# Kernel optimization log

Measured on AMD Instinct MI355X. Metric: run time of the kernel, lower is better.

## Reference

```python
import jax, jax.numpy as jnp
import numpy as np
import math

N_NODES = 50000
N_EDGES = 800000
D = 128        # in_channels == out_channels
H = 8          # num_heads
HD = D // H    # head_dim = 16
ED = 32        # edge_dim


def setup_inputs() -> dict:
    key = jax.random.key(0)
    ks = jax.random.split(key, 16)
    s = 1.0 / math.sqrt(D)
    se = 1.0 / math.sqrt(ED)
    return {
        "x": jax.random.normal(ks[0], (N_NODES, D), jnp.float32),
        "edge_index": jax.random.randint(ks[1], (2, N_EDGES), 0, N_NODES, jnp.int64),
        "edge_attr": jax.random.normal(ks[2], (N_EDGES, ED), jnp.float32),
        "Wq": jax.random.normal(ks[3], (D, D), jnp.float32) * s,
        "bq": jnp.zeros((D,), jnp.float32),
        "Wk": jax.random.normal(ks[4], (D, D), jnp.float32) * s,
        "bk": jnp.zeros((D,), jnp.float32),
        "Wv": jax.random.normal(ks[5], (D, D), jnp.float32) * s,
        "bv": jnp.zeros((D,), jnp.float32),
        "We": jax.random.normal(ks[6], (ED, H), jnp.float32) * se,
        "be": jnp.zeros((H,), jnp.float32),
        "Wo": jax.random.normal(ks[7], (D, D), jnp.float32) * s,
        "bo": jnp.zeros((D,), jnp.float32),
        "gamma": jnp.ones((D,), jnp.float32),
        "beta": jnp.zeros((D,), jnp.float32),
    }


def reference(x, edge_index, edge_attr, Wq, bq, Wk, bk, Wv, bv, We, be, Wo, bo, gamma, beta):
    n = x.shape[0]
    residual = x
    # node-wise projections -> [N, H, HD]
    q = (x @ Wq + bq).reshape(n, H, HD)
    k = (x @ Wk + bk).reshape(n, H, HD)
    v = (x @ Wv + bv).reshape(n, H, HD)
    src = edge_index[0]
    dst = edge_index[1]
    # edge-wise gather + dot-product attention score [E, H]
    score = jnp.einsum('ehd,ehd->eh', q[dst], k[src]) / math.sqrt(HD)
    score = score + edge_attr @ We + be
    # segmented (per-destination-node) stable softmax
    m = jax.ops.segment_max(score, dst, num_segments=n)          # [N, H]
    exp_s = jnp.exp(score - m[dst])                              # [E, H]
    ssum = jax.ops.segment_sum(exp_s, dst, num_segments=n)      # [N, H]
    attn = exp_s / (ssum[dst] + 1e-8)                            # [E, H]
    # weighted message scatter-add
    msg = attn[..., None] * v[src]                               # [E, H, HD]
    out = jax.ops.segment_sum(msg, dst, num_segments=n)          # [N, H, HD]
    out = out.reshape(n, D) @ Wo + bo
    # residual + layer norm (eps=1e-5, as nn.LayerNorm default)
    h = out + residual
    mu = h.mean(-1, keepdims=True)
    var = ((h - mu) ** 2).mean(-1, keepdims=True)
    return (h - mu) / jnp.sqrt(var + 1e-5) * gamma + beta
```

## Files before the change

### kernel.cpp

```cpp
#include <hip/hip_runtime.h>

#define DD 128
#define HH 8
#define HDIM 16
#define EDIM 32
#define CAP 64

typedef short short8_t __attribute__((ext_vector_type(8)));
typedef float f32x4 __attribute__((ext_vector_type(4)));

__device__ inline ushort f2bf(float f) {
    unsigned u = __float_as_uint(f);
    unsigned r = (u + 0x7fffu + ((u >> 16) & 1u)) >> 16;
    return (ushort)r;
}
__device__ inline float bf2f(ushort u) { return __uint_as_float(((unsigned)u) << 16); }

__global__ __launch_bounds__(256) void k_prep_w(
    const float* __restrict__ Wq, const float* __restrict__ Wk,
    const float* __restrict__ Wv, const float* __restrict__ Wo,
    ushort* __restrict__ wt)
{
    __shared__ ushort tw[128][136];
    const float* Ws[4] = {Wq, Wk, Wv, Wo};
    const float* W = Ws[blockIdx.x];
    const int t = threadIdx.x;
    for (int idx = t; idx < DD * DD; idx += 256) {
        int k = idx >> 7, c = idx & 127;
        tw[c][k] = f2bf(W[idx]);
    }
    __syncthreads();
    for (int u = t; u < 2048; u += 256) {
        int col = u >> 4, c8 = (u & 15) * 8;
        *(uint4*)&wt[((size_t)blockIdx.x * 128 + col) * 128 + c8] = *(const uint4*)&tw[col][c8];
    }
}

__global__ __launch_bounds__(256) void k_cvt_x(const float* __restrict__ x, ushort* __restrict__ xb, int total8) {
    int i = blockIdx.x * 256 + threadIdx.x;
    if (i >= total8) return;
    float4 a = *(const float4*)&x[(size_t)i * 8];
    float4 b = *(const float4*)&x[(size_t)i * 8 + 4];
    ushort o[8] = {f2bf(a.x), f2bf(a.y), f2bf(a.z), f2bf(a.w),
                   f2bf(b.x), f2bf(b.y), f2bf(b.z), f2bf(b.w)};
    *(uint4*)&xb[(size_t)i * 8] = *(const uint4*)o;
}

__global__ __launch_bounds__(256) void k_qkv(
    const ushort* __restrict__ xb, const ushort* __restrict__ wt,
    const float* __restrict__ bq, const float* __restrict__ bk, const float* __restrict__ bv,
    ushort* __restrict__ qb, ushort* __restrict__ kv, int N)
{
    __shared__ ushort xs[64][136];
    const int t = threadIdx.x;
    const int base = blockIdx.x * 64;

    for (int u = t; u < 1024; u += 256) {
        int r = u >> 4, c8 = (u & 15) * 8;
        int n = base + r;
        uint4 val = (n < N) ? *(const uint4*)&xb[(size_t)n * DD + c8] : make_uint4(0u, 0u, 0u, 0u);
        *(uint4*)&xs[r][c8] = val;
    }
    __syncthreads();

    const int lane = t & 63, w = t >> 6;
    const int lr = lane & 15, g = lane >> 4;
    const int node = base + w * 16 + lr;
    const bool valid = node < N;

    short8_t xf[4];
    #pragma unroll
    for (int ks = 0; ks < 4; ++ks)
        xf[ks] = *(const short8_t*)&xs[w * 16 + lr][ks * 32 + g * 8];

    const float* biases[3] = {bq, bk, bv};
    #pragma unroll
    for (int m = 0; m < 3; ++m) {
        f32x4 acc[8];
        #pragma unroll
        for (int rt = 0; rt < 8; ++rt) acc[rt] = (f32x4){0.f, 0.f, 0.f, 0.f};
        #pragma unroll
        for (int ks = 0; ks < 4; ++ks) {
            #pragma unroll
            for (int rt = 0; rt < 8; ++rt) {
                short8_t wf = *(const short8_t*)&wt[((size_t)m * 128 + rt * 16 + lr) * 128 + ks * 32 + g * 8];
                acc[rt] = __builtin_amdgcn_mfma_f32_16x16x32_bf16(wf, xf[ks], acc[rt], 0, 0, 0);
            }
        }
        if (valid) {
            #pragma unroll
            for (int rt = 0; rt < 8; ++rt) {
                int col = rt * 16 + g * 4;
                float4 b4 = *(const float4*)&biases[m][col];
                ushort o[4] = {f2bf(acc[rt][0] + b4.x), f2bf(acc[rt][1] + b4.y),
                               f2bf(acc[rt][2] + b4.z), f2bf(acc[rt][3] + b4.w)};
                if (m == 0) *(uint2*)&qb[(size_t)node * DD + col] = *(const uint2*)o;
                else        *(uint2*)&kv[(size_t)node * 256 + (m == 1 ? 0 : 128) + col] = *(const uint2*)o;
            }
        }
    }
}

__global__ __launch_bounds__(256) void k_edge(
    const int* __restrict__ ei, const float* __restrict__ edge_attr,
    const float* __restrict__ We, const float* __restrict__ be,
    int E, int N, int* __restrict__ cnt,
    int2* __restrict__ pe, ushort* __restrict__ escore_e)
{
    __shared__ float wel[EDIM * HH];
    __shared__ float bel[HH];
    int t = threadIdx.x;
    for (int i = t; i < EDIM * HH; i += 256) wel[i] = We[i];
    if (t < HH) bel[t] = be[t];
    __syncthreads();

    int e = blockIdx.x * 256 + t;
    if (e >= E) return;
    int dst = ei[E + e];
    int src = ei[e];

    float acc[HH];
    #pragma unroll
    for (int h = 0; h < HH; ++h) acc[h] = bel[h];
    #pragma unroll
    for (int c = 0; c < EDIM; c += 4) {
        float4 a4 = *(const float4*)&edge_attr[(size_t)e * EDIM + c];
        float av[4] = {a4.x, a4.y, a4.z, a4.w};
        #pragma unroll
        for (int cc = 0; cc < 4; ++cc)
            #pragma unroll
            for (int h = 0; h < HH; ++h)
                acc[h] += av[cc] * wel[(c + cc) * HH + h];
    }
    ushort o[8];
    #pragma unroll
    for (int h = 0; h < HH; ++h) o[h] = f2bf(acc[h]);
    *(uint4*)&escore_e[(size_t)e * 8] = *(const uint4*)o;

    if ((unsigned)dst < (unsigned)N) {
        int pos = atomicAdd(&cnt[dst], 1);
        if (pos < CAP)
            pe[(size_t)dst * CAP + pos] = make_int2(((unsigned)src < (unsigned)N) ? src : 0, e);
    }
}

__global__ __launch_bounds__(256) void k_agg(
    const ushort* __restrict__ qb, const ushort* __restrict__ kv,
    const int* __restrict__ cnt, const int2* __restrict__ pe,
    const ushort* __restrict__ escore_e,
    ushort* __restrict__ aggb, int N)
{
    int node = blockIdx.x * 4 + (threadIdx.x >> 6);
    if (node >= N) return;
    int lane = threadIdx.x & 63;
    int h = lane & 7, j = lane >> 3;

    float qr[HDIM];
    {
        uint4 qa = *(const uint4*)&qb[(size_t)node * DD + h * 16];
        uint4 qc = *(const uint4*)&qb[(size_t)node * DD + h * 16 + 8];
        unsigned ua[4] = {qa.x, qa.y, qa.z, qa.w};
        unsigned ub[4] = {qc.x, qc.y, qc.z, qc.w};
        #pragma unroll
        for (int i = 0; i < 4; ++i) {
            qr[2*i]     = __uint_as_float(ua[i] << 16);
            qr[2*i + 1] = __uint_as_float(ua[i] & 0xffff0000u);
            qr[8 + 2*i]     = __uint_as_float(ub[i] << 16);
            qr[8 + 2*i + 1] = __uint_as_float(ub[i] & 0xffff0000u);
        }
    }

    int deg = cnt[node];
    if (deg > CAP) deg = CAP;
    const size_t base = (size_t)node * CAP;

    float acc[HDIM];
    #pragma unroll
    for (int d = 0; d < HDIM; ++d) acc[d] = 0.f;
    float denom = 0.f;

    int tt = j;
    for (; tt + 8 < deg; tt += 16) {
        int2 r0 = pe[base + tt];
        int2 r1 = pe[base + tt + 8];
        int s0 = r0.x, s1 = r1.x;
        float e0 = bf2f(escore_e[(size_t)r0.y * 8 + h]);
        float e1 = bf2f(escore_e[(size_t)r1.y * 8 + h]);
        const uint4* kp0 = (const uint4*)&kv[(size_t)s0 * 256 + h * 16];
        const uint4* kp1 = (const uint4*)&kv[(size_t)s1 * 256 + h * 16];
        uint4 ka0 = kp0[0], kb0 = kp0[1];
        uint4 ka1 = kp1[0], kb1 = kp1[1];
        const uint4* vp0 = (const uint4*)&kv[(size_t)s0 * 256 + 128 + h * 16];
        const uint4* vp1 = (const uint4*)&kv[(size_t)s1 * 256 + 128 + h * 16];
        uint4 va0 = vp0[0], vb0 = vp0[1];
        uint4 va1 = vp1[0], vb1 = vp1[1];

        float kf0[16], kf1[16], vf0[16], vf1[16];
        {
            unsigned ua[4] = {ka0.x, ka0.y, ka0.z, ka0.w};
            unsigned ub[4] = {kb0.x, kb0.y, kb0.z, kb0.w};
            #pragma unroll
            for (int i = 0; i < 4; ++i) {
                kf0[2*i]     = __uint_as_float(ua[i] << 16);
                kf0[2*i + 1] = __uint_as_float(ua[i] & 0xffff0000u);
                kf0[8 + 2*i]     = __uint_as_float(ub[i] << 16);
                kf0[8 + 2*i + 1] = __uint_as_float(ub[i] & 0xffff0000u);
            }
        }
        {
            unsigned ua[4] = {ka1.x, ka1.y, ka1.z, ka1.w};
            unsigned ub[4] = {kb1.x, kb1.y, kb1.z, kb1.w};
            #pragma unroll
            for (int i = 0; i < 4; ++i) {
                kf1[2*i]     = __uint_as_float(ua[i] << 16);
                kf1[2*i + 1] = __uint_as_float(ua[i] & 0xffff0000u);
                kf1[8 + 2*i]     = __uint_as_float(ub[i] << 16);
                kf1[8 + 2*i + 1] = __uint_as_float(ub[i] & 0xffff0000u);
            }
        }
        {
            unsigned ua[4] = {va0.x, va0.y, va0.z, va0.w};
            unsigned ub[4] = {vb0.x, vb0.y, vb0.z, vb0.w};
            #pragma unroll
            for (int i = 0; i < 4; ++i) {
                vf0[2*i]     = __uint_as_float(ua[i] << 16);
                vf0[2*i + 1] = __uint_as_float(ua[i] & 0xffff0000u);
                vf0[8 + 2*i]     = __uint_as_float(ub[i] << 16);
                vf0[8 + 2*i + 1] = __uint_as_float(ub[i] & 0xffff0000u);
            }
        }
        {
            unsigned ua[4] = {va1.x, va1.y, va1.z, va1.w};
            unsigned ub[4] = {vb1.x, vb1.y, vb1.z, vb1.w};
            #pragma unroll
            for (int i = 0; i < 4; ++i) {
                vf1[2*i]     = __uint_as_float(ua[i] << 16);
                vf1[2*i + 1] = __uint_as_float(ua[i] & 0xffff0000u);
                vf1[8 + 2*i]     = __uint_as_float(ub[i] << 16);
                vf1[8 + 2*i + 1] = __uint_as_float(ub[i] & 0xffff0000u);
            }
        }
        float qk0 = 0.f, qk1 = 0.f;
        #pragma unroll
        for (int d = 0; d < HDIM; ++d) { qk0 += qr[d] * kf0[d]; qk1 += qr[d] * kf1[d]; }
        float w0 = __expf(e0 + qk0 * 0.25f);
        float w1 = __expf(e1 + qk1 * 0.25f);
        denom += w0 + w1;
        #pragma unroll
        for (int d = 0; d < HDIM; ++d) acc[d] += w0 * vf0[d] + w1 * vf1[d];
    }
    if (tt < deg) {
        int2 r0 = pe[base + tt];
        int s0 = r0.x;
        float e0 = bf2f(escore_e[(size_t)r0.y * 8 + h]);
        const uint4* kp0 = (const uint4*)&kv[(size_t)s0 * 256 + h * 16];
        uint4 ka0 = kp0[0], kb0 = kp0[1];
        const uint4* vp0 = (const uint4*)&kv[(size_t)s0 * 256 + 128 + h * 16];
        uint4 va0 = vp0[0], vb0 = vp0[1];
        float kf0[16], vf0[16];
        {
            unsigned ua[4] = {ka0.x, ka0.y, ka0.z, ka0.w};
            unsigned ub[4] = {kb0.x, kb0.y, kb0.z, kb0.w};
            #pragma unroll
            for (int i = 0; i < 4; ++i) {
                kf0[2*i]     = __uint_as_float(ua[i] << 16);
                kf0[2*i + 1] = __uint_as_float(ua[i] & 0xffff0000u);
                kf0[8 + 2*i]     = __uint_as_float(ub[i] << 16);
                kf0[8 + 2*i + 1] = __uint_as_float(ub[i] & 0xffff0000u);
            }
        }
        {
            unsigned ua[4] = {va0.x, va0.y, va0.z, va0.w};
            unsigned ub[4] = {vb0.x, vb0.y, vb0.z, vb0.w};
            #pragma unroll
            for (int i = 0; i < 4; ++i) {
                vf0[2*i]     = __uint_as_float(ua[i] << 16);
                vf0[2*i + 1] = __uint_as_float(ua[i] & 0xffff0000u);
                vf0[8 + 2*i]     = __uint_as_float(ub[i] << 16);
                vf0[8 + 2*i + 1] = __uint_as_float(ub[i] & 0xffff0000u);
            }
        }
        float qk0 = 0.f;
        #pragma unroll
        for (int d = 0; d < HDIM; ++d) qk0 += qr[d] * kf0[d];
        float w0 = __expf(e0 + qk0 * 0.25f);
        denom += w0;
        #pragma unroll
        for (int d = 0; d < HDIM; ++d) acc[d] += w0 * vf0[d];
    }

    #pragma unroll
    for (int m = 8; m < 64; m <<= 1) {
        denom += __shfl_xor(denom, m, 64);
        #pragma unroll
        for (int d = 0; d < HDIM; ++d) acc[d] += __shfl_xor(acc[d], m, 64);
    }

    if (j == 0) {
        float inv = 1.f / (denom + 1e-8f);
        unsigned uu[8];
        #pragma unroll
        for (int i = 0; i < 8; ++i) {
            unsigned lo = f2bf(acc[2*i] * inv);
            unsigned hi = f2bf(acc[2*i + 1] * inv);
            uu[i] = lo | (hi << 16);
        }
        *(uint4*)&aggb[(size_t)node * DD + h * 16]     = *(const uint4*)&uu[0];
        *(uint4*)&aggb[(size_t)node * DD + h * 16 + 8] = *(const uint4*)&uu[4];
    }
}

__global__ __launch_bounds__(256) void k_final(
    const ushort* __restrict__ aggb, const ushort* __restrict__ wto,
    const float* __restrict__ x, const float* __restrict__ bo,
    const float* __restrict__ gamma, const float* __restrict__ beta,
    float* __restrict__ out, int N)
{
    __shared__ ushort as_[64][136];
    const int t = threadIdx.x;
    const int base = blockIdx.x * 64;

    for (int u = t; u < 1024; u += 256) {
        int r = u >> 4, c8 = (u & 15) * 8;
        int n = base + r;
        uint4 val = (n < N) ? *(const uint4*)&aggb[(size_t)n * DD + c8] : make_uint4(0u, 0u, 0u, 0u);
        *(uint4*)&as_[r][c8] = val;
    }
    __syncthreads();

    const int lane = t & 63, w = t >> 6;
    const int lr = lane & 15, g = lane >> 4;
    const int node = base + w * 16 + lr;
    const bool valid = node < N;

    short8_t af[4];
    #pragma unroll
    for (int ks = 0; ks < 4; ++ks)
        af[ks] = *(const short8_t*)&as_[w * 16 + lr][ks * 32 + g * 8];

    f32x4 acc[8];
    #pragma unroll
    for (int rt = 0; rt < 8; ++rt) acc[rt] = (f32x4){0.f, 0.f, 0.f, 0.f};
    #pragma unroll
    for (int ks = 0; ks < 4; ++ks) {
        #pragma unroll
        for (int rt = 0; rt < 8; ++rt) {
            short8_t wf = *(const short8_t*)&wto[((size_t)rt * 16 + lr) * 128 + ks * 32 + g * 8];
            acc[rt] = __builtin_amdgcn_mfma_f32_16x16x32_bf16(wf, af[ks], acc[rt], 0, 0, 0);
        }
    }

    float s = 0.f, sq = 0.f;
    #pragma unroll
    for (int rt = 0; rt < 8; ++rt) {
        int col = rt * 16 + g * 4;
        float4 b4 = *(const float4*)&bo[col];
        float4 xr = valid ? *(const float4*)&x[(size_t)node * DD + col] : make_float4(0.f, 0.f, 0.f, 0.f);
        float y0 = acc[rt][0] + b4.x + xr.x;
        float y1 = acc[rt][1] + b4.y + xr.y;
        float y2 = acc[rt][2] + b4.z + xr.z;
        float y3 = acc[rt][3] + b4.w + xr.w;
        acc[rt][0] = y0; acc[rt][1] = y1; acc[rt][2] = y2; acc[rt][3] = y3;
        s += y0 + y1 + y2 + y3;
        sq += y0 * y0 + y1 * y1 + y2 * y2 + y3 * y3;
    }
    s  += __shfl_xor(s, 16, 64);  sq += __shfl_xor(sq, 16, 64);
    s  += __shfl_xor(s, 32, 64);  sq += __shfl_xor(sq, 32, 64);

    float mu = s * (1.f / 128.f);
    float var = sq * (1.f / 128.f) - mu * mu;
    float rstd = rsqrtf(var + 1e-5f);

    if (valid) {
        #pragma unroll
        for (int rt = 0; rt < 8; ++rt) {
            int col = rt * 16 + g * 4;
            float4 g4 = *(const float4*)&gamma[col];
            float4 e4 = *(const float4*)&beta[col];
            float4 o;
            o.x = (acc[rt][0] - mu) * rstd * g4.x + e4.x;
            o.y = (acc[rt][1] - mu) * rstd * g4.y + e4.y;
            o.z = (acc[rt][2] - mu) * rstd * g4.z + e4.z;
            o.w = (acc[rt][3] - mu) * rstd * g4.w + e4.w;
            *(float4*)&out[(size_t)node * DD + col] = o;
        }
    }
}

extern "C" void kernel_launch(void* const* d_in, const int* in_sizes, int n_in,
                              void* d_out, int out_size, void* d_ws, size_t ws_size,
                              hipStream_t stream) {
    const float* x     = (const float*)d_in[0];
    const int*   ei    = (const int*)d_in[1];
    const float* ea    = (const float*)d_in[2];
    const float* Wq    = (const float*)d_in[3];
    const float* bq    = (const float*)d_in[4];
    const float* Wk    = (const float*)d_in[5];
    const float* bk    = (const float*)d_in[6];
    const float* Wv    = (const float*)d_in[7];
    const float* bv    = (const float*)d_in[8];
    const float* We    = (const float*)d_in[9];
    const float* be    = (const float*)d_in[10];
    const float* Wo    = (const float*)d_in[11];
    const float* bo    = (const float*)d_in[12];
    const float* gamma = (const float*)d_in[13];
    const float* beta  = (const float*)d_in[14];
    float* out = (float*)d_out;

    const int N = in_sizes[0] / DD;
    const int E = in_sizes[2] / EDIM;

    int2*   pe       = (int2*)d_ws;
    ushort* qb       = (ushort*)(pe + (size_t)N * CAP);
    ushort* kv       = qb + (size_t)N * DD;
    ushort* xb       = kv + (size_t)N * 256;
    ushort* aggb     = xb + (size_t)N * DD;
    ushort* wt       = aggb + (size_t)N * DD;
    ushort* escore_e = wt + 4 * 128 * 128;
    int*    cnt      = (int*)(escore_e + (size_t)E * 8);

    hipMemsetAsync(cnt, 0, (size_t)N * sizeof(int), stream);

    const int nodeTiles64 = (N + 63) / 64;
    const int edgeBlocks  = (E + 255) / 256;
    const int aggBlocks   = (N + 3) / 4;
    const int total8      = N * DD / 8;
    const int cvtBlocks   = (total8 + 255) / 256;

    k_cvt_x<<<cvtBlocks, 256, 0, stream>>>(x, xb, total8);
    k_prep_w<<<4, 256, 0, stream>>>(Wq, Wk, Wv, Wo, wt);
    k_qkv<<<nodeTiles64, 256, 0, stream>>>(xb, wt, bq, bk, bv, qb, kv, N);
    k_edge<<<edgeBlocks, 256, 0, stream>>>(ei, ea, We, be, E, N, cnt, pe, escore_e);
    k_agg<<<aggBlocks, 256, 0, stream>>>(qb, kv, cnt, pe, escore_e, aggb, N);
    k_final<<<nodeTiles64, 256, 0, stream>>>(aggb, wt + 3 * 128 * 128, x, bo, gamma, beta, out, N);
}
```

Before: 229.1 us.

## Fuse x conversion into QKV and merge edge and QKV kernels

```diff
diff --git a/kernel.cpp b/kernel.cpp
--- a/kernel.cpp
+++ b/kernel.cpp
@@ -36,30 +36,71 @@
     }
 }
 
-__global__ __launch_bounds__(256) void k_cvt_x(const float* __restrict__ x, ushort* __restrict__ xb, int total8) {
-    int i = blockIdx.x * 256 + threadIdx.x;
-    if (i >= total8) return;
-    float4 a = *(const float4*)&x[(size_t)i * 8];
-    float4 b = *(const float4*)&x[(size_t)i * 8 + 4];
-    ushort o[8] = {f2bf(a.x), f2bf(a.y), f2bf(a.z), f2bf(a.w),
-                   f2bf(b.x), f2bf(b.y), f2bf(b.z), f2bf(b.w)};
-    *(uint4*)&xb[(size_t)i * 8] = *(const uint4*)o;
-}
-
-__global__ __launch_bounds__(256) void k_qkv(
-    const ushort* __restrict__ xb, const ushort* __restrict__ wt,
+__global__ __launch_bounds__(256) void k_mega(
+    const int* __restrict__ ei, const float* __restrict__ edge_attr,
+    const float* __restrict__ We, const float* __restrict__ be,
+    int E, int N, int* __restrict__ cnt,
+    int2* __restrict__ pe, ushort* __restrict__ escore_e,
+    const float* __restrict__ x, const ushort* __restrict__ wt,
     const float* __restrict__ bq, const float* __restrict__ bk, const float* __restrict__ bv,
-    ushort* __restrict__ qb, ushort* __restrict__ kv, int N)
+    ushort* __restrict__ qb, ushort* __restrict__ kv,
+    int edgeBlocks)
 {
     __shared__ ushort xs[64][136];
     const int t = threadIdx.x;
-    const int base = blockIdx.x * 64;
+
+    if (blockIdx.x < edgeBlocks) {
+        float* wel = (float*)&xs[0][0];
+        float* bel = wel + EDIM * HH;
+        for (int i = t; i < EDIM * HH; i += 256) wel[i] = We[i];
+        if (t < HH) bel[t] = be[t];
+        __syncthreads();
+
+        int e = blockIdx.x * 256 + t;
+        if (e >= E) return;
+        int dst = ei[E + e];
+        int src = ei[e];
+
+        float acc[HH];
+        #pragma unroll
+        for (int h = 0; h < HH; ++h) acc[h] = bel[h];
+        #pragma unroll
+        for (int c = 0; c < EDIM; c += 4) {
+            float4 a4 = *(const float4*)&edge_attr[(size_t)e * EDIM + c];
+            float av[4] = {a4.x, a4.y, a4.z, a4.w};
+            #pragma unroll
+            for (int cc = 0; cc < 4; ++cc)
+                #pragma unroll
+                for (int h = 0; h < HH; ++h)
+                    acc[h] += av[cc] * wel[(c + cc) * HH + h];
+        }
+        ushort o[8];
+        #pragma unroll
+        for (int h = 0; h < HH; ++h) o[h] = f2bf(acc[h]);
+        *(uint4*)&escore_e[(size_t)e * 8] = *(const uint4*)o;
+
+        if ((unsigned)dst < (unsigned)N) {
+            int pos = atomicAdd(&cnt[dst], 1);
+            if (pos < CAP)
+                pe[(size_t)dst * CAP + pos] = make_int2(((unsigned)src < (unsigned)N) ? src : 0, e);
+        }
+        return;
+    }
+
+    const int base = (blockIdx.x - edgeBlocks) * 64;
 
     for (int u = t; u < 1024; u += 256) {
         int r = u >> 4, c8 = (u & 15) * 8;
         int n = base + r;
-        uint4 val = (n < N) ? *(const uint4*)&xb[(size_t)n * DD + c8] : make_uint4(0u, 0u, 0u, 0u);
-        *(uint4*)&xs[r][c8] = val;
+        if (n < N) {
+            float4 a = *(const float4*)&x[(size_t)n * DD + c8];
+            float4 b = *(const float4*)&x[(size_t)n * DD + c8 + 4];
+            ushort o[8] = {f2bf(a.x), f2bf(a.y), f2bf(a.z), f2bf(a.w),
+                           f2bf(b.x), f2bf(b.y), f2bf(b.z), f2bf(b.w)};
+            *(uint4*)&xs[r][c8] = *(const uint4*)o;
+        } else {
+            *(uint4*)&xs[r][c8] = make_uint4(0u, 0u, 0u, 0u);
+        }
     }
     __syncthreads();
 
@@ -98,49 +139,6 @@
                 else        *(uint2*)&kv[(size_t)node * 256 + (m == 1 ? 0 : 128) + col] = *(const uint2*)o;
             }
         }
-    }
-}
-
-__global__ __launch_bounds__(256) void k_edge(
-    const int* __restrict__ ei, const float* __restrict__ edge_attr,
-    const float* __restrict__ We, const float* __restrict__ be,
-    int E, int N, int* __restrict__ cnt,
-    int2* __restrict__ pe, ushort* __restrict__ escore_e)
-{
-    __shared__ float wel[EDIM * HH];
-    __shared__ float bel[HH];
-    int t = threadIdx.x;
-    for (int i = t; i < EDIM * HH; i += 256) wel[i] = We[i];
-    if (t < HH) bel[t] = be[t];
-    __syncthreads();
-
-    int e = blockIdx.x * 256 + t;
-    if (e >= E) return;
-    int dst = ei[E + e];
-    int src = ei[e];
-
-    float acc[HH];
-    #pragma unroll
-    for (int h = 0; h < HH; ++h) acc[h] = bel[h];
-    #pragma unroll
-    for (int c = 0; c < EDIM; c += 4) {
-        float4 a4 = *(const float4*)&edge_attr[(size_t)e * EDIM + c];
-        float av[4] = {a4.x, a4.y, a4.z, a4.w};
-        #pragma unroll
-        for (int cc = 0; cc < 4; ++cc)
-            #pragma unroll
-            for (int h = 0; h < HH; ++h)
-                acc[h] += av[cc] * wel[(c + cc) * HH + h];
-    }
-    ushort o[8];
-    #pragma unroll
-    for (int h = 0; h < HH; ++h) o[h] = f2bf(acc[h]);
-    *(uint4*)&escore_e[(size_t)e * 8] = *(const uint4*)o;
-
-    if ((unsigned)dst < (unsigned)N) {
-        int pos = atomicAdd(&cnt[dst], 1);
-        if (pos < CAP)
-            pe[(size_t)dst * CAP + pos] = make_int2(((unsigned)src < (unsigned)N) ? src : 0, e);
     }
 }
 
@@ -413,8 +411,7 @@
     int2*   pe       = (int2*)d_ws;
     ushort* qb       = (ushort*)(pe + (size_t)N * CAP);
     ushort* kv       = qb + (size_t)N * DD;
-    ushort* xb       = kv + (size_t)N * 256;
-    ushort* aggb     = xb + (size_t)N * DD;
+    ushort* aggb     = kv + (size_t)N * 256;
     ushort* wt       = aggb + (size_t)N * DD;
     ushort* escore_e = wt + 4 * 128 * 128;
     int*    cnt      = (int*)(escore_e + (size_t)E * 8);
@@ -424,13 +421,11 @@
     const int nodeTiles64 = (N + 63) / 64;
     const int edgeBlocks  = (E + 255) / 256;
     const int aggBlocks   = (N + 3) / 4;
-    const int total8      = N * DD / 8;
-    const int cvtBlocks   = (total8 + 255) / 256;
-
-    k_cvt_x<<<cvtBlocks, 256, 0, stream>>>(x, xb, total8);
+
     k_prep_w<<<4, 256, 0, stream>>>(Wq, Wk, Wv, Wo, wt);
-    k_qkv<<<nodeTiles64, 256, 0, stream>>>(xb, wt, bq, bk, bv, qb, kv, N);
-    k_edge<<<edgeBlocks, 256, 0, stream>>>(ei, ea, We, be, E, N, cnt, pe, escore_e);
+    k_mega<<<edgeBlocks + nodeTiles64, 256, 0, stream>>>(
+        ei, ea, We, be, E, N, cnt, pe, escore_e,
+        x, wt, bq, bk, bv, qb, kv, edgeBlocks);
     k_agg<<<aggBlocks, 256, 0, stream>>>(qb, kv, cnt, pe, escore_e, aggb, N);
     k_final<<<nodeTiles64, 256, 0, stream>>>(aggb, wt + 3 * 128 * 128, x, bo, gamma, beta, out, N);
 }
```

Measured after the change: 212.5 us. -7.2%, faster.
